# Optimization experiments

Measured on AMD Instinct MI355X. Metric: run time of the kernel, lower is better.

Reference implementation:

```python
import jax, jax.numpy as jnp
import numpy as np

NV, NS = 100000, 50000
DG, DS, H, OUT = 5, 6, 64, 8
EVV, EH, EIN, ESS = 1_000_000, 1_000_000, 500_000, 1_000_000


def _segsum(data, idx, n):
    return jax.ops.segment_sum(data, idx, num_segments=n)


def _edge_index(key, e, n_src, n_dst):
    k1, k2 = jax.random.split(key)
    return jnp.stack([
        jax.random.randint(k1, (e,), 0, n_src),
        jax.random.randint(k2, (e,), 0, n_dst),
    ]).astype(jnp.int64)


def setup_inputs() -> dict:
    key = jax.random.key(0)
    ks = jax.random.split(key, 16)
    s = 0.1
    inp = {
        "game_x": jax.random.normal(ks[0], (NV, DG), jnp.float32),
        "state_x": jax.random.normal(ks[1], (NS, DS), jnp.float32),
        "edge_index_v_v": _edge_index(ks[2], EVV, NV, NV),
        "edge_index_history_v_s": _edge_index(ks[3], EH, NV, NS),
        "edge_attr_history_v_s": jax.random.uniform(ks[4], (EH,), jnp.float32),
        "edge_index_in_v_s": _edge_index(ks[5], EIN, NV, NS),
        "edge_index_s_s": _edge_index(ks[6], ESS, NS, NS),
        # TAGConv(5, H, K=2): K+1 bias-free linears + bias
        "tag1_W": jax.random.normal(ks[7], (3, DG, H), jnp.float32) * s,
        "tag1_b": jnp.zeros((H,), jnp.float32),
        # TAGConv(H, H, K=3)
        "tag2_W": jax.random.normal(ks[8], (4, H, H), jnp.float32) * s,
        "tag2_b": jnp.zeros((H,), jnp.float32),
        # GraphConv((-1,-1), H): lin_rel (bias) + lin_root (no bias)
        "gc_W_rel": jax.random.normal(ks[9], (H, H), jnp.float32) * s,
        "gc_b": jnp.zeros((H,), jnp.float32),
        "gc_W_root": jax.random.normal(ks[10], (DS, H), jnp.float32) * s,
        # SAGEConv((-1,-1), H): lin_l (bias) + lin_r (no bias), mean aggr
        "sage_W_l": jax.random.normal(ks[11], (H, H), jnp.float32) * s,
        "sage_b_l": jnp.zeros((H,), jnp.float32),
        "sage_W_r": jax.random.normal(ks[12], (H, H), jnp.float32) * s,
        "lin_W": jax.random.normal(ks[13], (H, OUT), jnp.float32) * s,
        "lin_b": jnp.zeros((OUT,), jnp.float32),
    }
    return inp


def _tag_conv(x, edge_index, W, b):
    # TAGConv with gcn_norm (no self-loops): out = sum_k lin_k(A_hat^k x) + b
    n = x.shape[0]
    src, dst = edge_index[0], edge_index[1]
    deg = _segsum(jnp.ones(src.shape[0], x.dtype), dst, n)
    dinv = jnp.where(deg > 0, jax.lax.rsqrt(jnp.maximum(deg, 1e-12)), 0.0)
    norm = dinv[src] * dinv[dst]  # [E]
    out = x @ W[0]
    h = x
    for k in range(1, W.shape[0]):  # fixed, small K
        h = _segsum(h[src] * norm[:, None], dst, n)
        out = out + h @ W[k]
    return out + b


def _forward(game_x, state_x, edge_attr_history_v_s,
             tag1_W, tag1_b, tag2_W, tag2_b,
             gc_W_rel, gc_b, gc_W_root,
             sage_W_l, sage_b_l, sage_W_r, lin_W, lin_b,
             edge_index_v_v, edge_index_history_v_s,
             edge_index_in_v_s, edge_index_s_s):
    ns = state_x.shape[0]
    gx = jax.nn.relu(_tag_conv(game_x, edge_index_v_v, tag1_W, tag1_b))
    # GraphConv bipartite with edge weights: lin_rel(sum w*x_j) + lin_root(x_dst)
    src, dst = edge_index_history_v_s[0], edge_index_history_v_s[1]
    agg = _segsum(gx[src] * edge_attr_history_v_s[:, None], dst, ns)
    sx = jax.nn.relu(agg @ gc_W_rel + gc_b + state_x @ gc_W_root)
    # SAGEConv bipartite, mean aggr: lin_l(mean x_j) + lin_r(x_dst)
    src, dst = edge_index_in_v_s[0], edge_index_in_v_s[1]
    ssum = _segsum(gx[src], dst, ns)
    cnt = _segsum(jnp.ones(src.shape[0], gx.dtype), dst, ns)
    mean = ssum / jnp.maximum(cnt, 1.0)[:, None]
    sx = jax.nn.relu(mean @ sage_W_l + sage_b_l + sx @ sage_W_r)
    sx = jax.nn.relu(_tag_conv(sx, edge_index_s_s, tag2_W, tag2_b))
    return sx @ lin_W + lin_b


def reference(game_x, state_x, edge_index_v_v, edge_index_history_v_s,
              edge_attr_history_v_s, edge_index_in_v_s, edge_index_s_s,
              tag1_W, tag1_b, tag2_W, tag2_b, gc_W_rel, gc_b, gc_W_root,
              sage_W_l, sage_b_l, sage_W_r, lin_W, lin_b):
    return _forward(game_x, state_x, edge_attr_history_v_s,
                    tag1_W, tag1_b, tag2_W, tag2_b,
                    gc_W_rel, gc_b, gc_W_root,
                    sage_W_l, sage_b_l, sage_W_r, lin_W, lin_b,
                    edge_index_v_v, edge_index_history_v_s,
                    edge_index_in_v_s, edge_index_s_s)
```

## Files before the change

### kernel.cpp

```cpp
#include <hip/hip_runtime.h>

#define BLK 256
#define ACH 4096

__device__ __forceinline__ float bcast(float v, int l) {
    return __int_as_float(__builtin_amdgcn_readlane(__float_as_int(v), l));
}
__device__ __forceinline__ unsigned short f2bf(float f) {
    unsigned u = __float_as_uint(f);
    return (unsigned short)((u + 0x7FFFu + ((u >> 16) & 1u)) >> 16);
}
__device__ __forceinline__ float bf2f(unsigned short b) {
    return __uint_as_float(((unsigned)b) << 16);
}

typedef __attribute__((ext_vector_type(8))) short bf16x8;
typedef __attribute__((ext_vector_type(4))) float f32x4;

__device__ __forceinline__ void split8s(const float* p, float s, bf16x8& h, bf16x8& l) {
    #pragma unroll
    for (int j = 0; j < 8; j++) {
        float v = p[j] * s;
        unsigned short hb = f2bf(v);
        h[j] = (short)hb;
        l[j] = (short)f2bf(v - bf2f(hb));
    }
}
__device__ __forceinline__ void loadWsplit(const float* W, int kbase, int col,
                                           bf16x8& h, bf16x8& l) {
    #pragma unroll
    for (int j = 0; j < 8; j++) {
        float v = W[(size_t)(kbase + j) * 64 + col];
        unsigned short hb = f2bf(v);
        h[j] = (short)hb;
        l[j] = (short)f2bf(v - bf2f(hb));
    }
}


__global__ void k_binA1(const int* __restrict__ vd, const int* __restrict__ hd,
                        const int* __restrict__ id_, const int* __restrict__ sd,
                        int* __restrict__ Tv, int* __restrict__ Th,
                        int* __restrict__ Ti, int* __restrict__ Ts,
                        int ncv, int nch, int nci, int ncs,
                        int nbv_, int nbs_, int Ev, int Eh, int Ei, int Es) {
    __shared__ int cnt[512];
    int blk = blockIdx.x, t = threadIdx.x;
    const int* dd; int* T; int c, nc, nb, E, sf;
    if (blk < ncv)                 { dd = vd;  T = Tv; c = blk;               nc = ncv; nb = nbv_; E = Ev; sf = 8; }
    else if (blk < ncv + nch)      { dd = hd;  T = Th; c = blk - ncv;         nc = nch; nb = nbs_; E = Eh; sf = 7; }
    else if (blk < ncv + nch + nci){ dd = id_; T = Ti; c = blk - ncv - nch;   nc = nci; nb = nbs_; E = Ei; sf = 7; }
    else                           { dd = sd;  T = Ts; c = blk - ncv - nch - nci; nc = ncs; nb = nbs_; E = Es; sf = 7; }
    cnt[t] = 0; cnt[t + 256] = 0;
    __syncthreads();
    int p0 = c * ACH, p1 = min(E, p0 + ACH);
    for (int p = p0 + t; p < p1; p += 256) atomicAdd(&cnt[dd[p] >> sf], 1);
    __syncthreads();
    for (int b = t; b < nb; b += 256) T[(size_t)b * nc + c] = cnt[b];
}

__global__ void k_sb2(int* __restrict__ T, int* __restrict__ bsum,
                      int L0, int L1, int L2, int L3,
                      int nB0, int nB1, int nB2, int nB3) {
    __shared__ int sh[256];
    int blk = blockIdx.x;
    int lb, off, L;
    if (blk < nB0)                  { lb = blk;                 off = 0;            L = L0; }
    else if (blk < nB0 + nB1)       { lb = blk - nB0;           off = L0;           L = L1; }
    else if (blk < nB0 + nB1 + nB2) { lb = blk - nB0 - nB1;     off = L0 + L1;      L = L2; }
    else                            { lb = blk - nB0 - nB1 - nB2; off = L0 + L1 + L2; L = L3; }
    int i = lb * 256 + threadIdx.x;
    int v = (i < L) ? T[off + i] : 0;
    sh[threadIdx.x] = v; __syncthreads();
    for (int o2 = 1; o2 < 256; o2 <<= 1) {
        int tmp = (threadIdx.x >= o2) ? sh[threadIdx.x - o2] : 0;
        __syncthreads();
        sh[threadIdx.x] += tmp; __syncthreads();
    }
    if (i < L) T[off + i] = sh[threadIdx.x] - v;
    if (threadIdx.x == 255) bsum[blk] = sh[255];
}

__global__ void k_st2(int* __restrict__ bsum, int nB0, int nB1, int nB2, int nB3) {
    __shared__ int sh[1024];
    int g = blockIdx.x;
    int off = (g == 0) ? 0 : (g == 1) ? nB0 : (g == 2) ? nB0 + nB1 : nB0 + nB1 + nB2;
    int nb  = (g == 0) ? nB0 : (g == 1) ? nB1 : (g == 2) ? nB2 : nB3;
    int tid = threadIdx.x;
    int v = (tid < nb) ? bsum[off + tid] : 0;
    sh[tid] = v; __syncthreads();
    for (int o2 = 1; o2 < 1024; o2 <<= 1) {
        int t = (tid >= o2) ? sh[tid - o2] : 0;
        __syncthreads();
        sh[tid] += t; __syncthreads();
    }
    if (tid < nb) bsum[off + tid] = sh[tid] - v;
}

__global__ void k_sa2(int* __restrict__ T, const int* __restrict__ bsum,
                      int L0, int L1, int L2, int L3,
                      int nB0, int nB1, int nB2, int nB3) {
    int blk = blockIdx.x;
    int lb, off, L;
    if (blk < nB0)                  { lb = blk;                 off = 0;            L = L0; }
    else if (blk < nB0 + nB1)       { lb = blk - nB0;           off = L0;           L = L1; }
    else if (blk < nB0 + nB1 + nB2) { lb = blk - nB0 - nB1;     off = L0 + L1;      L = L2; }
    else                            { lb = blk - nB0 - nB1 - nB2; off = L0 + L1 + L2; L = L3; }
    int i = lb * 256 + threadIdx.x;
    if (i < L) T[off + i] += bsum[blk];
}

__global__ __launch_bounds__(512)
void k_binA2a(const int* __restrict__ vs, const int* __restrict__ vd,
              const int* __restrict__ is_, const int* __restrict__ id_,
              const int* __restrict__ ss_, const int* __restrict__ sd,
              const int* __restrict__ Tv, const int* __restrict__ Ti,
              const int* __restrict__ Ts,
              unsigned* __restrict__ vvbin, unsigned* __restrict__ inbin,
              unsigned* __restrict__ ssbin,
              int ncv, int nci, int ncs, int nbv_, int nbs_,
              int Ev, int Ei, int Es) {
    __shared__ int gbase[512], lscan[512], lcur[512];
    __shared__ unsigned sval[ACH];
    __shared__ int sdst[ACH];
    int blk = blockIdx.x, t = threadIdx.x;
    const int *srcp, *dstp, *T; unsigned* bin; int c, nc, nb, E, sf;
    if (blk < ncv)            { srcp = vs;  dstp = vd;  T = Tv; bin = vvbin; c = blk;             nc = ncv; nb = nbv_; E = Ev; sf = 8; }
    else if (blk < ncv + nci) { srcp = is_; dstp = id_; T = Ti; bin = inbin; c = blk - ncv;       nc = nci; nb = nbs_; E = Ei; sf = 7; }
    else                      { srcp = ss_; dstp = sd;  T = Ts; bin = ssbin; c = blk - ncv - nci; nc = ncs; nb = nbs_; E = Es; sf = 7; }
    int msk = (1 << sf) - 1;
    int p0 = c * ACH, p1 = min(E, p0 + ACH);
    if (t < nb) gbase[t] = T[(size_t)t * nc + c];
    lcur[t] = 0;
    int myS[8], myD[8];
    #pragma unroll
    for (int i = 0; i < 8; i++) {
        int p = p0 + t + i * 512;
        if (p < p1) { myS[i] = srcp[p]; myD[i] = dstp[p]; }
        else myD[i] = -1;
    }
    __syncthreads();
    #pragma unroll
    for (int i = 0; i < 8; i++)
        if (myD[i] >= 0) atomicAdd(&lcur[myD[i] >> sf], 1);
    __syncthreads();
    int v = lcur[t];
    lscan[t] = v;
    __syncthreads();
    for (int off = 1; off < 512; off <<= 1) {
        int tmp = (t >= off) ? lscan[t - off] : 0;
        __syncthreads();
        lscan[t] += tmp;
        __syncthreads();
    }
    int excl = lscan[t] - v;
    __syncthreads();
    lscan[t] = excl;
    lcur[t] = 0;
    __syncthreads();
    #pragma unroll
    for (int i = 0; i < 8; i++) {
        if (myD[i] < 0) continue;
        int b = myD[i] >> sf;
        int r = atomicAdd(&lcur[b], 1);
        int pos = lscan[b] + r;
        sval[pos] = ((unsigned)myS[i] << sf) | (unsigned)(myD[i] & msk);
        sdst[pos] = gbase[b] + r;
    }
    __syncthreads();
    int cntE = p1 - p0;
    for (int q = t; q < cntE; q += 512) bin[sdst[q]] = sval[q];
}

__global__ __launch_bounds__(512)
void k_binA2h(const int* __restrict__ hs, const int* __restrict__ hd,
              const float* __restrict__ hw, const int* __restrict__ Th,
              int2* __restrict__ hbin, int nch, int nbs_, int Eh) {
    __shared__ int gbase[512], lscan[512], lcur[512];
    __shared__ unsigned sval[ACH];
    __shared__ int sdst[ACH];
    __shared__ float swt[ACH];
    int c = blockIdx.x, t = threadIdx.x;
    const int sf = 7, msk = 127;
    int p0 = c * ACH, p1 = min(Eh, p0 + ACH);
    if (t < nbs_) gbase[t] = Th[(size_t)t * nch + c];
    lcur[t] = 0;
    int myS[8], myD[8]; float myW[8];
    #pragma unroll
    for (int i = 0; i < 8; i++) {
        int p = p0 + t + i * 512;
        if (p < p1) { myS[i] = hs[p]; myD[i] = hd[p]; myW[i] = hw[p]; }
        else myD[i] = -1;
    }
    __syncthreads();
    #pragma unroll
    for (int i = 0; i < 8; i++)
        if (myD[i] >= 0) atomicAdd(&lcur[myD[i] >> sf], 1);
    __syncthreads();
    int v = lcur[t];
    lscan[t] = v;
    __syncthreads();
    for (int off = 1; off < 512; off <<= 1) {
        int tmp = (t >= off) ? lscan[t - off] : 0;
        __syncthreads();
        lscan[t] += tmp;
        __syncthreads();
    }
    int excl = lscan[t] - v;
    __syncthreads();
    lscan[t] = excl;
    lcur[t] = 0;
    __syncthreads();
    #pragma unroll
    for (int i = 0; i < 8; i++) {
        if (myD[i] < 0) continue;
        int b = myD[i] >> sf;
        int r = atomicAdd(&lcur[b], 1);
        int pos = lscan[b] + r;
        sval[pos] = ((unsigned)myS[i] << sf) | (unsigned)(myD[i] & msk);
        sdst[pos] = gbase[b] + r;
        swt[pos] = myW[i];
    }
    __syncthreads();
    int cntE = p1 - p0;
    for (int q = t; q < cntE; q += 512)
        hbin[sdst[q]] = make_int2((int)sval[q], __float_as_int(swt[q]));
}

__global__ void k_binB(const unsigned* __restrict__ vvbin, const int2* __restrict__ hbin,
                       const unsigned* __restrict__ inbin, const unsigned* __restrict__ ssbin,
                       const int* __restrict__ Tv, const int* __restrict__ Th,
                       const int* __restrict__ Ti, const int* __restrict__ Ts,
                       int* __restrict__ rv, int* __restrict__ rh,
                       int* __restrict__ ri, int* __restrict__ rs,
                       float* __restrict__ dinv_v, float* __restrict__ dinv_s,
                       int* __restrict__ vvsrc, int2* __restrict__ hsw,
                       int* __restrict__ insrc, int* __restrict__ sssrc,
                       int ncv, int nch, int nci, int ncs,
                       int nbv_, int nbs_, int nv, int ns,
                       int Ev, int Eh, int Ei, int Es) {
    __shared__ int cnt[256]; __shared__ int pre[256]; __shared__ int cur[256];
    int blk = blockIdx.x, t = threadIdx.x;
    int g, b, nb, nc, sf, n, E; const int* T; int* rp;
    if (blk < nbv_)                 { g = 0; b = blk;                 nb = nbv_; nc = ncv; sf = 8; n = nv; E = Ev; T = Tv; rp = rv; }
    else if (blk < nbv_ + nbs_)     { g = 1; b = blk - nbv_;          nb = nbs_; nc = nch; sf = 7; n = ns; E = Eh; T = Th; rp = rh; }
    else if (blk < nbv_ + 2 * nbs_) { g = 2; b = blk - nbv_ - nbs_;   nb = nbs_; nc = nci; sf = 7; n = ns; E = Ei; T = Ti; rp = ri; }
    else                            { g = 3; b = blk - nbv_ - 2 * nbs_; nb = nbs_; nc = ncs; sf = 7; n = ns; E = Es; T = Ts; rp = rs; }
    int W = 1 << sf, msk = W - 1;
    int e0 = T[(size_t)b * nc];
    int e1 = (b + 1 < nb) ? T[(size_t)(b + 1) * nc] : E;
    cnt[t] = 0; __syncthreads();
    for (int p = e0 + t; p < e1; p += 256) {
        unsigned pk = (g == 1) ? (unsigned)hbin[p].x
                    : (g == 0) ? vvbin[p] : (g == 2) ? inbin[p] : ssbin[p];
        atomicAdd(&cnt[pk & msk], 1);
    }
    __syncthreads();
    int v = cnt[t];
    pre[t] = v; __syncthreads();
    for (int o2 = 1; o2 < 256; o2 <<= 1) {
        int tmp = (t >= o2) ? pre[t - o2] : 0;
        __syncthreads();
        pre[t] += tmp; __syncthreads();
    }
    int excl = pre[t] - v;
    int d = b * W + t;
    if (t < W && d < n) {
        rp[d] = e0 + excl;
        if (g == 0)      dinv_v[d] = v > 0 ? rsqrtf((float)v) : 0.f;
        else if (g == 3) dinv_s[d] = v > 0 ? rsqrtf((float)v) : 0.f;
    }
    cur[t] = e0 + excl;
    __syncthreads();
    for (int p = e0 + t; p < e1; p += 256) {
        if (g == 1) {
            int2 r = hbin[p];
            unsigned pk = (unsigned)r.x;
            int pos = atomicAdd(&cur[pk & msk], 1);
            hsw[pos] = make_int2((int)(pk >> sf), r.y);
        } else {
            unsigned pk = (g == 0) ? vvbin[p] : (g == 2) ? inbin[p] : ssbin[p];
            int pos = atomicAdd(&cur[pk & msk], 1);
            int sv = (int)(pk >> sf);
            if (g == 0)      vvsrc[pos] = sv;
            else if (g == 2) insrc[pos] = sv;
            else             sssrc[pos] = sv;
        }
    }
    if (b == 0 && t == 0) rp[n] = E;
}


__global__ void k_pack5(const float* __restrict__ x, const float* __restrict__ dinv,
                        float* __restrict__ P, int n) {
    int i = blockIdx.x * blockDim.x + threadIdx.x;
    if (i >= n) return;
    const float* xp = x + (size_t)i * 5;
    float4 a = make_float4(xp[0], xp[1], xp[2], xp[3]);
    float4 b = make_float4(xp[4], dinv[i], 0.f, 0.f);
    ((float4*)P)[(size_t)i * 2]     = a;
    ((float4*)P)[(size_t)i * 2 + 1] = b;
}

__global__ void k_gather5p(const float* __restrict__ Pin, const int* __restrict__ rowptr,
                           const int* __restrict__ csr_src, float* __restrict__ Pout, int n) {
    int d = blockIdx.x * blockDim.x + threadIdx.x;
    if (d >= n) return;
    int b = rowptr[d], e = rowptr[d + 1];
    float dd = Pin[(size_t)d * 8 + 5];
    float a0 = 0, a1 = 0, a2 = 0, a3 = 0, a4 = 0;
    int p = b;
    for (; p + 4 <= e; p += 4) {
        int s0 = csr_src[p], s1 = csr_src[p+1], s2 = csr_src[p+2], s3 = csr_src[p+3];
        float4 x0a = ((const float4*)Pin)[(size_t)s0 * 2], x0b = ((const float4*)Pin)[(size_t)s0 * 2 + 1];
        float4 x1a = ((const float4*)Pin)[(size_t)s1 * 2], x1b = ((const float4*)Pin)[(size_t)s1 * 2 + 1];
        float4 x2a = ((const float4*)Pin)[(size_t)s2 * 2], x2b = ((const float4*)Pin)[(size_t)s2 * 2 + 1];
        float4 x3a = ((const float4*)Pin)[(size_t)s3 * 2], x3b = ((const float4*)Pin)[(size_t)s3 * 2 + 1];
        float w0 = dd * x0b.y, w1 = dd * x1b.y, w2 = dd * x2b.y, w3 = dd * x3b.y;
        a0 += x0a.x*w0 + x1a.x*w1 + x2a.x*w2 + x3a.x*w3;
        a1 += x0a.y*w0 + x1a.y*w1 + x2a.y*w2 + x3a.y*w3;
        a2 += x0a.z*w0 + x1a.z*w1 + x2a.z*w2 + x3a.z*w3;
        a3 += x0a.w*w0 + x1a.w*w1 + x2a.w*w2 + x3a.w*w3;
        a4 += x0b.x*w0 + x1b.x*w1 + x2b.x*w2 + x3b.x*w3;
    }
    for (; p < e; p++) {
        int s = csr_src[p];
        float4 xa = ((const float4*)Pin)[(size_t)s * 2], xb = ((const float4*)Pin)[(size_t)s * 2 + 1];
        float w = dd * xb.y;
        a0 += xa.x*w; a1 += xa.y*w; a2 += xa.z*w; a3 += xa.w*w; a4 += xb.x*w;
    }
    ((float4*)Pout)[(size_t)d * 2]     = make_float4(a0, a1, a2, a3);
    ((float4*)Pout)[(size_t)d * 2 + 1] = make_float4(a4, dd, 0.f, 0.f);
}

template<int MODE, bool OUTBF>
__global__ void k_gather64(const unsigned short* __restrict__ xbf, const int* __restrict__ rowptr,
                           const int* __restrict__ csr_src, const int2* __restrict__ csr_sw,
                           const float* __restrict__ dinv, void* __restrict__ outp, int n) {
    int wid = (int)(((long long)blockIdx.x * blockDim.x + threadIdx.x) >> 6);
    if (wid >= n) return;
    int lane = threadIdx.x & 63;
    int g = lane >> 4, q = lane & 15;
    int b = rowptr[wid], e = rowptr[wid + 1];
    float dd = (MODE == 2) ? dinv[wid] : 0.f;
    float4 acc = make_float4(0.f, 0.f, 0.f, 0.f);
    int p = b + g;
    for (; p + 12 < e; p += 16) {
        int s0, s1, s2, s3;
        float w0 = 1.f, w1 = 1.f, w2 = 1.f, w3 = 1.f;
        if (MODE == 1) {
            int2 e0 = csr_sw[p], e1 = csr_sw[p+4], e2 = csr_sw[p+8], e3 = csr_sw[p+12];
            s0 = e0.x; w0 = __int_as_float(e0.y);
            s1 = e1.x; w1 = __int_as_float(e1.y);
            s2 = e2.x; w2 = __int_as_float(e2.y);
            s3 = e3.x; w3 = __int_as_float(e3.y);
        } else {
            s0 = csr_src[p]; s1 = csr_src[p+4]; s2 = csr_src[p+8]; s3 = csr_src[p+12];
            if (MODE == 2) {
                w0 = dd * dinv[s0]; w1 = dd * dinv[s1];
                w2 = dd * dinv[s2]; w3 = dd * dinv[s3];
            }
        }
        ushort4 u0 = ((const ushort4*)(xbf + (size_t)s0 * 64))[q];
        ushort4 u1 = ((const ushort4*)(xbf + (size_t)s1 * 64))[q];
        ushort4 u2 = ((const ushort4*)(xbf + (size_t)s2 * 64))[q];
        ushort4 u3 = ((const ushort4*)(xbf + (size_t)s3 * 64))[q];
        acc.x += bf2f(u0.x)*w0 + bf2f(u1.x)*w1 + bf2f(u2.x)*w2 + bf2f(u3.x)*w3;
        acc.y += bf2f(u0.y)*w0 + bf2f(u1.y)*w1 + bf2f(u2.y)*w2 + bf2f(u3.y)*w3;
        acc.z += bf2f(u0.z)*w0 + bf2f(u1.z)*w1 + bf2f(u2.z)*w2 + bf2f(u3.z)*w3;
        acc.w += bf2f(u0.w)*w0 + bf2f(u1.w)*w1 + bf2f(u2.w)*w2 + bf2f(u3.w)*w3;
    }
    for (; p < e; p += 4) {
        int s; float w = 1.f;
        if (MODE == 1) { int2 e0 = csr_sw[p]; s = e0.x; w = __int_as_float(e0.y); }
        else { s = csr_src[p]; if (MODE == 2) w = dd * dinv[s]; }
        ushort4 u = ((const ushort4*)(xbf + (size_t)s * 64))[q];
        acc.x += bf2f(u.x)*w; acc.y += bf2f(u.y)*w;
        acc.z += bf2f(u.z)*w; acc.w += bf2f(u.w)*w;
    }
    #pragma unroll
    for (int off = 16; off < 64; off <<= 1) {
        acc.x += __shfl_xor(acc.x, off, 64);
        acc.y += __shfl_xor(acc.y, off, 64);
        acc.z += __shfl_xor(acc.z, off, 64);
        acc.w += __shfl_xor(acc.w, off, 64);
    }
    if (g == 0) {
        if (OUTBF) {
            ushort4 ov;
            ov.x = f2bf(acc.x); ov.y = f2bf(acc.y); ov.z = f2bf(acc.z); ov.w = f2bf(acc.w);
            ((ushort4*)outp)[(size_t)wid * 16 + q] = ov;
        } else {
            ((float4*)outp)[(size_t)wid * 16 + q] = acc;
        }
    }
}


__global__ __launch_bounds__(256)
void k_sage_mf(const float* __restrict__ ssum, const int* __restrict__ rp,
               const float* __restrict__ sx, const float* __restrict__ Wl,
               const float* __restrict__ Wr, const float* __restrict__ bl,
               unsigned short* __restrict__ out, int n) {
    int wv = (int)(((long long)blockIdx.x * blockDim.x + threadIdx.x) >> 6);
    int lane = threadIdx.x & 63;
    int r0 = wv * 32;
    if (r0 >= n) return;
    int lm = lane & 15, g = lane >> 4;
    bf16x8 axh[2][2], axl[2][2], ayh[2][2], ayl[2][2];
    #pragma unroll
    for (int mt = 0; mt < 2; mt++) {
        int row = r0 + mt * 16 + lm; if (row >= n) row = n - 1;
        float cnt = (float)(rp[row + 1] - rp[row]);
        float rs = 1.f / fmaxf(cnt, 1.f);
        #pragma unroll
        for (int kh = 0; kh < 2; kh++) {
            split8s(ssum + (size_t)row * 64 + kh * 32 + g * 8, rs,  axh[mt][kh], axl[mt][kh]);
            split8s(sx   + (size_t)row * 64 + kh * 32 + g * 8, 1.f, ayh[mt][kh], ayl[mt][kh]);
        }
    }
    #pragma unroll
    for (int nt = 0; nt < 4; nt++) {
        int col = nt * 16 + lm;
        bf16x8 blh[2], bll[2], brh[2], brl[2];
        #pragma unroll
        for (int kh = 0; kh < 2; kh++) {
            loadWsplit(Wl, kh * 32 + g * 8, col, blh[kh], bll[kh]);
            loadWsplit(Wr, kh * 32 + g * 8, col, brh[kh], brl[kh]);
        }
        #pragma unroll
        for (int mt = 0; mt < 2; mt++) {
            f32x4 acc = {0.f, 0.f, 0.f, 0.f};
            #pragma unroll
            for (int kh = 0; kh < 2; kh++) {
                acc = __builtin_amdgcn_mfma_f32_16x16x32_bf16(axh[mt][kh], blh[kh], acc, 0, 0, 0);
                acc = __builtin_amdgcn_mfma_f32_16x16x32_bf16(axl[mt][kh], blh[kh], acc, 0, 0, 0);
                acc = __builtin_amdgcn_mfma_f32_16x16x32_bf16(axh[mt][kh], bll[kh], acc, 0, 0, 0);
                acc = __builtin_amdgcn_mfma_f32_16x16x32_bf16(ayh[mt][kh], brh[kh], acc, 0, 0, 0);
                acc = __builtin_amdgcn_mfma_f32_16x16x32_bf16(ayl[mt][kh], brh[kh], acc, 0, 0, 0);
                acc = __builtin_amdgcn_mfma_f32_16x16x32_bf16(ayh[mt][kh], brl[kh], acc, 0, 0, 0);
            }
            #pragma unroll
            for (int r = 0; r < 4; r++) {
                int row = r0 + mt * 16 + g * 4 + r;
                if (row < n)
                    out[(size_t)row * 64 + col] = f2bf(fmaxf(bl[col] + acc[r], 0.f));
            }
        }
    }
}

__global__ __launch_bounds__(256)
void k_gc_mf(const float* __restrict__ agg, const float* __restrict__ st,
             const float* __restrict__ Wrel, const float* __restrict__ Wroot,
             const float* __restrict__ b, float* __restrict__ out, int n) {
    int wv = (int)(((long long)blockIdx.x * blockDim.x + threadIdx.x) >> 6);
    int lane = threadIdx.x & 63;
    int r0 = wv * 32;
    if (r0 >= n) return;
    int lm = lane & 15, g = lane >> 4;
    bf16x8 axh[2][2], axl[2][2], arh[2], arl[2];
    #pragma unroll
    for (int mt = 0; mt < 2; mt++) {
        int row = r0 + mt * 16 + lm; if (row >= n) row = n - 1;
        #pragma unroll
        for (int kh = 0; kh < 2; kh++)
            split8s(agg + (size_t)row * 64 + kh * 32 + g * 8, 1.f, axh[mt][kh], axl[mt][kh]);
        #pragma unroll
        for (int j = 0; j < 8; j++) {
            int k = g * 8 + j;
            float v = (k < 6) ? st[(size_t)row * 6 + k] : 0.f;
            unsigned short hb = f2bf(v);
            arh[mt][j] = (short)hb;
            arl[mt][j] = (short)f2bf(v - bf2f(hb));
        }
    }
    #pragma unroll
    for (int nt = 0; nt < 4; nt++) {
        int col = nt * 16 + lm;
        bf16x8 bh[2], blo[2], brh, brl;
        #pragma unroll
        for (int kh = 0; kh < 2; kh++) loadWsplit(Wrel, kh * 32 + g * 8, col, bh[kh], blo[kh]);
        #pragma unroll
        for (int j = 0; j < 8; j++) {
            int k = g * 8 + j;
            float v = (k < 6) ? Wroot[(size_t)k * 64 + col] : 0.f;
            unsigned short hb = f2bf(v);
            brh[j] = (short)hb;
            brl[j] = (short)f2bf(v - bf2f(hb));
        }
        #pragma unroll
        for (int mt = 0; mt < 2; mt++) {
            f32x4 acc = {0.f, 0.f, 0.f, 0.f};
            #pragma unroll
            for (int kh = 0; kh < 2; kh++) {
                acc = __builtin_amdgcn_mfma_f32_16x16x32_bf16(axh[mt][kh], bh[kh],  acc, 0, 0, 0);
                acc = __builtin_amdgcn_mfma_f32_16x16x32_bf16(axl[mt][kh], bh[kh],  acc, 0, 0, 0);
                acc = __builtin_amdgcn_mfma_f32_16x16x32_bf16(axh[mt][kh], blo[kh], acc, 0, 0, 0);
            }
            acc = __builtin_amdgcn_mfma_f32_16x16x32_bf16(arh[mt], brh, acc, 0, 0, 0);
            acc = __builtin_amdgcn_mfma_f32_16x16x32_bf16(arl[mt], brh, acc, 0, 0, 0);
            acc = __builtin_amdgcn_mfma_f32_16x16x32_bf16(arh[mt], brl, acc, 0, 0, 0);
            #pragma unroll
            for (int r = 0; r < 4; r++) {
                int row = r0 + mt * 16 + g * 4 + r;
                if (row < n)
                    out[(size_t)row * 64 + col] = fmaxf(b[col] + acc[r], 0.f);
            }
        }
    }
}

__global__ __launch_bounds__(256)
void k_tagmm(const unsigned short* __restrict__ x0, const unsigned short* __restrict__ x1,
             const unsigned short* __restrict__ x2, const unsigned short* __restrict__ x3,
             const float* __restrict__ W4, const float* __restrict__ tb,
             const float* __restrict__ lW, const float* __restrict__ lb,
             float* __restrict__ out, int n) {
    __shared__ float lds[4][32][64];
    int tid = threadIdx.x;
    int wv = (int)(((long long)blockIdx.x * blockDim.x + tid) >> 6);
    int w = (tid >> 6) & 3;
    int lane = tid & 63;
    int lm = lane & 15, g = lane >> 4;
    int r0 = wv * 32;
    bool active = (r0 < n);
    int r0c = active ? r0 : 0;
    const unsigned short* xs[4] = {x0, x1, x2, x3};
    f32x4 acc[2][4];
    #pragma unroll
    for (int mt = 0; mt < 2; mt++)
        #pragma unroll
        for (int nt = 0; nt < 4; nt++) acc[mt][nt] = (f32x4){0.f, 0.f, 0.f, 0.f};
    #pragma unroll
    for (int inp = 0; inp < 4; inp++) {
        const unsigned short* xp = xs[inp];
        const float* W = W4 + inp * 4096;
        bf16x8 a[2][2];
        #pragma unroll
        for (int mt = 0; mt < 2; mt++) {
            int row = r0c + mt * 16 + lm; if (row >= n) row = n - 1;
            #pragma unroll
            for (int kh = 0; kh < 2; kh++)
                a[mt][kh] = *(const bf16x8*)(xp + (size_t)row * 64 + kh * 32 + g * 8);
        }
        #pragma unroll
        for (int nt = 0; nt < 4; nt++) {
            int col = nt * 16 + lm;
            bf16x8 bh[2], blo[2];
            #pragma unroll
            for (int kh = 0; kh < 2; kh++) loadWsplit(W, kh * 32 + g * 8, col, bh[kh], blo[kh]);
            #pragma unroll
            for (int mt = 0; mt < 2; mt++) {
                #pragma unroll
                for (int kh = 0; kh < 2; kh++) {
                    acc[mt][nt] = __builtin_amdgcn_mfma_f32_16x16x32_bf16(a[mt][kh], bh[kh],  acc[mt][nt], 0, 0, 0);
                    acc[mt][nt] = __builtin_amdgcn_mfma_f32_16x16x32_bf16(a[mt][kh], blo[kh], acc[mt][nt], 0, 0, 0);
                }
            }
        }
    }
    #pragma unroll
    for (int mt = 0; mt < 2; mt++)
        #pragma unroll
        for (int nt = 0; nt < 4; nt++) {
            int col = nt * 16 + lm;
            float bias = tb[col];
            #pragma unroll
            for (int r = 0; r < 4; r++)
                lds[w][mt * 16 + g * 4 + r][col] = fmaxf(bias + acc[mt][nt][r], 0.f);
        }
    __syncthreads();
    bf16x8 bh2[2], bl2[2];
    #pragma unroll
    for (int kh = 0; kh < 2; kh++) {
        #pragma unroll
        for (int j = 0; j < 8; j++) {
            int k = kh * 32 + g * 8 + j;
            float v = (lm < 8) ? lW[k * 8 + lm] : 0.f;
            unsigned short hb = f2bf(v);
            bh2[kh][j] = (short)hb;
            bl2[kh][j] = (short)f2bf(v - bf2f(hb));
        }
    }
    #pragma unroll
    for (int mt = 0; mt < 2; mt++) {
        bf16x8 ah[2], al[2];
        #pragma unroll
        for (int kh = 0; kh < 2; kh++) {
            #pragma unroll
            for (int j = 0; j < 8; j++) {
                float v = lds[w][mt * 16 + lm][kh * 32 + g * 8 + j];
                unsigned short hb = f2bf(v);
                ah[kh][j] = (short)hb;
                al[kh][j] = (short)f2bf(v - bf2f(hb));
            }
        }
        f32x4 oacc = {0.f, 0.f, 0.f, 0.f};
        #pragma unroll
        for (int kh = 0; kh < 2; kh++) {
            oacc = __builtin_amdgcn_mfma_f32_16x16x32_bf16(ah[kh], bh2[kh], oacc, 0, 0, 0);
            oacc = __builtin_amdgcn_mfma_f32_16x16x32_bf16(al[kh], bh2[kh], oacc, 0, 0, 0);
            oacc = __builtin_amdgcn_mfma_f32_16x16x32_bf16(ah[kh], bl2[kh], oacc, 0, 0, 0);
        }
        if (lm < 8) {
            #pragma unroll
            for (int r = 0; r < 4; r++) {
                int row = r0 + mt * 16 + g * 4 + r;
                if (active && row < n) out[(size_t)row * 8 + lm] = oacc[r] + lb[lm];
            }
        }
    }
}

__global__ __launch_bounds__(256, 4)
void k_tag1_w(const float* __restrict__ x, const float* __restrict__ h1,
              const float* __restrict__ h2, const float* __restrict__ W,
              const float* __restrict__ b, unsigned short* __restrict__ out, int n) {
    int wv = (int)(((long long)blockIdx.x * blockDim.x + threadIdx.x) >> 6);
    int lane = threadIdx.x & 63;
    int i0 = wv * 4;
    if (i0 >= n) return;
    float v[4], acc[4];
    #pragma unroll
    for (int r = 0; r < 4; r++) {
        int i = (i0 + r < n) ? i0 + r : n - 1;
        float t = 0.f;
        if (lane < 5)                     t = x [(size_t)i * 5 + lane];
        else if (lane >= 8 && lane < 13)  t = h1[(size_t)i * 8 + lane - 8];
        else if (lane >= 16 && lane < 21) t = h2[(size_t)i * 8 + lane - 16];
        v[r] = t;
        acc[r] = b[lane];
    }
    #pragma unroll
    for (int m = 0; m < 3; m++) {
        #pragma unroll
        for (int k = 0; k < 5; k++) {
            float wk = W[(m * 5 + k) * 64 + lane];
            #pragma unroll
            for (int r = 0; r < 4; r++) acc[r] += bcast(v[r], m * 8 + k) * wk;
        }
    }
    #pragma unroll
    for (int r = 0; r < 4; r++)
        if (i0 + r < n) out[(size_t)(i0 + r) * 64 + lane] = f2bf(fmaxf(acc[r], 0.f));
}

static inline unsigned gblk(long long n) { return (unsigned)((n + BLK - 1) / BLK); }
static inline unsigned gwv4(long long n) { return gblk(((n + 3) / 4) * 64); }
static inline unsigned gw32(long long n) { return gblk(((n + 31) / 32) * 64); }

extern "C" void kernel_launch(void* const* d_in, const int* in_sizes, int n_in,
                              void* d_out, int out_size, void* d_ws, size_t ws_size,
                              hipStream_t stream) {
    const float* game_x  = (const float*)d_in[0];
    const float* state_x = (const float*)d_in[1];
    const int*   ei_vv   = (const int*)d_in[2];
    const int*   ei_h    = (const int*)d_in[3];
    const float* ea_h    = (const float*)d_in[4];
    const int*   ei_in   = (const int*)d_in[5];
    const int*   ei_ss   = (const int*)d_in[6];
    const float* tag1_W  = (const float*)d_in[7];
    const float* tag1_b  = (const float*)d_in[8];
    const float* tag2_W  = (const float*)d_in[9];
    const float* tag2_b  = (const float*)d_in[10];
    const float* gc_Wrel = (const float*)d_in[11];
    const float* gc_b    = (const float*)d_in[12];
    const float* gc_Wroot= (const float*)d_in[13];
    const float* sage_Wl = (const float*)d_in[14];
    const float* sage_bl = (const float*)d_in[15];
    const float* sage_Wr = (const float*)d_in[16];
    const float* lin_W   = (const float*)d_in[17];
    const float* lin_b   = (const float*)d_in[18];

    const int NV  = in_sizes[0] / 5;
    const int NS  = in_sizes[1] / 6;
    const int EVV = in_sizes[2] / 2;
    const int EH  = in_sizes[3] / 2;
    const int EIN = in_sizes[5] / 2;
    const int ESS = in_sizes[6] / 2;

    const int *vv_s = ei_vv,  *vv_d = ei_vv + EVV;
    const int *h_s  = ei_h,   *h_d  = ei_h  + EH;
    const int *in_s = ei_in,  *in_d = ei_in + EIN;
    const int *ss_s = ei_ss,  *ss_d = ei_ss + ESS;

    const int ncv = (EVV + ACH - 1) / ACH;
    const int nch = (EH  + ACH - 1) / ACH;
    const int nci = (EIN + ACH - 1) / ACH;
    const int ncs = (ESS + ACH - 1) / ACH;
    const int nbv_ = (NV + 255) >> 8;
    const int nbs_ = (NS + 127) >> 7;
    const int Lv = nbv_ * ncv, Lh = nbs_ * nch, Li = nbs_ * nci, Ls = nbs_ * ncs;
    const int nB0 = (Lv + 255) / 256, nB1 = (Lh + 255) / 256,
              nB2 = (Li + 255) / 256, nB3 = (Ls + 255) / 256;

    float* wsf = (float*)d_ws;
    size_t o = 0;
    unsigned short* gx_bf = (unsigned short*)(wsf + o);
    o += (size_t)NV * 32;
    float* B1 = wsf + o; o += (size_t)NS * 64;
    float* B2 = wsf + o; o += (size_t)NS * 64;
    float* B4 = wsf + o; o += (size_t)NS * 32;
    float* B5 = wsf + o; o += (size_t)NS * 32;
    int*  vvsrc = (int*)(wsf + o); o += (size_t)EVV;
    int*  sssrc = (int*)(wsf + o); o += (size_t)ESS;
    int*  insrc = (int*)(wsf + o); o += (size_t)EIN;
    int2* hsw   = (int2*)(wsf + o); o += (size_t)EH * 2;
    int* T_all = (int*)(wsf + o); o += (size_t)(Lv + Lh + Li + Ls);
    int* bsum  = (int*)(wsf + o); o += 2048;
    int* rv = (int*)(wsf + o); o += (size_t)NV + 1;
    int* rh = (int*)(wsf + o); o += (size_t)NS + 1;
    int* ri = (int*)(wsf + o); o += (size_t)NS + 1;
    int* rs = (int*)(wsf + o); o += (size_t)NS + 1;
    float* dinv_v = wsf + o; o += (size_t)NV;
    float* dinv_s = wsf + o; o += (size_t)NS;

    int* Tv = T_all;
    int* Th = Tv + Lv;
    int* Ti = Th + Lh;
    int* Ts = Ti + Li;

    unsigned* vvbin = (unsigned*)B1;
    unsigned* inbin = vvbin + EVV;
    unsigned* ssbin = inbin + EIN;
    int2* hbin = (int2*)B2;

    unsigned short* hA_bf  = (unsigned short*)B1;
    unsigned short* hB_bf  = (unsigned short*)B2;
    unsigned short* hC_bf  = (unsigned short*)B5;
    unsigned short* sx2_bf = (unsigned short*)B4;
    float* P0 = B5;
    float* H1 = B4;
    float* H2 = B4 + (size_t)NV * 8;

    int nbins   = nbv_ + 3 * nbs_;
    int nBtot   = nB0 + nB1 + nB2 + nB3;
    k_binA1<<<ncv + nch + nci + ncs, 256, 0, stream>>>(vv_d, h_d, in_d, ss_d, Tv, Th, Ti, Ts,
                                         ncv, nch, nci, ncs, nbv_, nbs_,
                                         EVV, EH, EIN, ESS);
    k_sb2<<<nBtot, 256, 0, stream>>>(T_all, bsum, Lv, Lh, Li, Ls, nB0, nB1, nB2, nB3);
    k_st2<<<4, 1024, 0, stream>>>(bsum, nB0, nB1, nB2, nB3);
    k_sa2<<<nBtot, 256, 0, stream>>>(T_all, bsum, Lv, Lh, Li, Ls, nB0, nB1, nB2, nB3);
    k_binA2a<<<ncv + nci + ncs, 512, 0, stream>>>(vv_s, vv_d, in_s, in_d, ss_s, ss_d,
                                                  Tv, Ti, Ts, vvbin, inbin, ssbin,
                                                  ncv, nci, ncs, nbv_, nbs_,
                                                  EVV, EIN, ESS);
    k_binA2h<<<nch, 512, 0, stream>>>(h_s, h_d, ea_h, Th, hbin, nch, nbs_, EH);
    k_binB<<<nbins, 256, 0, stream>>>(vvbin, hbin, inbin, ssbin,
                                      Tv, Th, Ti, Ts,
                                      rv, rh, ri, rs, dinv_v, dinv_s,
                                      vvsrc, hsw, insrc, sssrc,
                                      ncv, nch, nci, ncs, nbv_, nbs_,
                                      NV, NS, EVV, EH, EIN, ESS);

    k_pack5<<<gblk(NV), BLK, 0, stream>>>(game_x, dinv_v, P0, NV);
    k_gather5p<<<gblk(NV), BLK, 0, stream>>>(P0, rv, vvsrc, H1, NV);
    k_gather5p<<<gblk(NV), BLK, 0, stream>>>(H1, rv, vvsrc, H2, NV);
    k_tag1_w<<<gwv4(NV), BLK, 0, stream>>>(game_x, H1, H2, tag1_W, tag1_b, gx_bf, NV);

    k_gather64<1, false><<<gblk((long long)NS * 64), BLK, 0, stream>>>(gx_bf, rh, nullptr, hsw, nullptr, B1, NS);
    k_gc_mf<<<gw32(NS), BLK, 0, stream>>>(B1, state_x, gc_Wrel, gc_Wroot, gc_b, B2, NS);

    k_gather64<0, false><<<gblk((long long)NS * 64), BLK, 0, stream>>>(gx_bf, ri, insrc, nullptr, nullptr, B1, NS);
    k_sage_mf<<<gw32(NS), BLK, 0, stream>>>(B1, ri, B2, sage_Wl, sage_Wr, sage_bl, sx2_bf, NS);

    k_gather64<2, true><<<gblk((long long)NS * 64), BLK, 0, stream>>>(sx2_bf, rs, sssrc, nullptr, dinv_s, hA_bf, NS);
    k_gather64<2, true><<<gblk((long long)NS * 64), BLK, 0, stream>>>(hA_bf, rs, sssrc, nullptr, dinv_s, hB_bf, NS);
    k_gather64<2, true><<<gblk((long long)NS * 64), BLK, 0, stream>>>(hB_bf, rs, sssrc, nullptr, dinv_s, hC_bf, NS);
    k_tagmm<<<gw32(NS), BLK, 0, stream>>>(sx2_bf, hA_bf, hB_bf, hC_bf,
                                          tag2_W, tag2_b, lin_W, lin_b,
                                          (float*)d_out, NS);
}
```

Before: 395.6 us.

## Fuse pack into binning, merge GC/SAGE gathers and matmuls into fewer kernels

Folds the game_x packing and dinv computation into the CSR-building k_binB kernel, removing k_pack5 and the dinv_v buffer. The history and in-edge gathers now run in a single launch (k_gatherBC), with the first half of the waves handling history and the second half in-edges. GraphConv and SAGE matmuls are fused into one kernel that keeps the intermediate state features in LDS instead of writing them to global memory. This cuts launch count and intermediate global traffic, at the cost of 32KB LDS per block, which may lower occupancy, and a block-wide sync.

New measurement: 411.4 us. 4.0% more time.

```diff
diff --git a/kernel.cpp b/kernel.cpp
--- a/kernel.cpp
+++ b/kernel.cpp
@@ -233,7 +233,8 @@
                        const int* __restrict__ Ti, const int* __restrict__ Ts,
                        int* __restrict__ rv, int* __restrict__ rh,
                        int* __restrict__ ri, int* __restrict__ rs,
-                       float* __restrict__ dinv_v, float* __restrict__ dinv_s,
+                       const float* __restrict__ gx5, float* __restrict__ P0,
+                       float* __restrict__ dinv_s,
                        int* __restrict__ vvsrc, int2* __restrict__ hsw,
                        int* __restrict__ insrc, int* __restrict__ sssrc,
                        int ncv, int nch, int nci, int ncs,
@@ -267,8 +268,14 @@
     int d = b * W + t;
     if (t < W && d < n) {
         rp[d] = e0 + excl;
-        if (g == 0)      dinv_v[d] = v > 0 ? rsqrtf((float)v) : 0.f;
-        else if (g == 3) dinv_s[d] = v > 0 ? rsqrtf((float)v) : 0.f;
+        if (g == 0) {
+            const float* xp = gx5 + (size_t)d * 5;
+            float di = v > 0 ? rsqrtf((float)v) : 0.f;
+            ((float4*)P0)[(size_t)d * 2]     = make_float4(xp[0], xp[1], xp[2], xp[3]);
+            ((float4*)P0)[(size_t)d * 2 + 1] = make_float4(xp[4], di, 0.f, 0.f);
+        } else if (g == 3) {
+            dinv_s[d] = v > 0 ? rsqrtf((float)v) : 0.f;
+        }
     }
     cur[t] = e0 + excl;
     __syncthreads();
@@ -290,17 +297,6 @@
     if (b == 0 && t == 0) rp[n] = E;
 }
 
-
-__global__ void k_pack5(const float* __restrict__ x, const float* __restrict__ dinv,
-                        float* __restrict__ P, int n) {
-    int i = blockIdx.x * blockDim.x + threadIdx.x;
-    if (i >= n) return;
-    const float* xp = x + (size_t)i * 5;
-    float4 a = make_float4(xp[0], xp[1], xp[2], xp[3]);
-    float4 b = make_float4(xp[4], dinv[i], 0.f, 0.f);
-    ((float4*)P)[(size_t)i * 2]     = a;
-    ((float4*)P)[(size_t)i * 2 + 1] = b;
-}
 
 __global__ void k_gather5p(const float* __restrict__ Pin, const int* __restrict__ rowptr,
                            const int* __restrict__ csr_src, float* __restrict__ Pout, int n) {
@@ -331,6 +327,75 @@
     }
     ((float4*)Pout)[(size_t)d * 2]     = make_float4(a0, a1, a2, a3);
     ((float4*)Pout)[(size_t)d * 2 + 1] = make_float4(a4, dd, 0.f, 0.f);
+}
+
+__global__ void k_gatherBC(const unsigned short* __restrict__ xbf,
+                           const int* __restrict__ rh, const int2* __restrict__ hsw,
+                           const int* __restrict__ ri, const int* __restrict__ insrc,
+                           float* __restrict__ aggH, float* __restrict__ aggI, int n) {
+    int wid = (int)(((long long)blockIdx.x * blockDim.x + threadIdx.x) >> 6);
+    if (wid >= 2 * n) return;
+    int lane = threadIdx.x & 63;
+    int g = lane >> 4, q = lane & 15;
+    float4 acc = make_float4(0.f, 0.f, 0.f, 0.f);
+    float* outp;
+    int row;
+    if (wid < n) {
+        row = wid;
+        int b = rh[row], e = rh[row + 1];
+        int p = b + g;
+        for (; p + 12 < e; p += 16) {
+            int2 e0 = hsw[p], e1 = hsw[p+4], e2 = hsw[p+8], e3 = hsw[p+12];
+            float w0 = __int_as_float(e0.y), w1 = __int_as_float(e1.y);
+            float w2 = __int_as_float(e2.y), w3 = __int_as_float(e3.y);
+            ushort4 u0 = ((const ushort4*)(xbf + (size_t)e0.x * 64))[q];
+            ushort4 u1 = ((const ushort4*)(xbf + (size_t)e1.x * 64))[q];
+            ushort4 u2 = ((const ushort4*)(xbf + (size_t)e2.x * 64))[q];
+            ushort4 u3 = ((const ushort4*)(xbf + (size_t)e3.x * 64))[q];
+            acc.x += bf2f(u0.x)*w0 + bf2f(u1.x)*w1 + bf2f(u2.x)*w2 + bf2f(u3.x)*w3;
+            acc.y += bf2f(u0.y)*w0 + bf2f(u1.y)*w1 + bf2f(u2.y)*w2 + bf2f(u3.y)*w3;
+            acc.z += bf2f(u0.z)*w0 + bf2f(u1.z)*w1 + bf2f(u2.z)*w2 + bf2f(u3.z)*w3;
+            acc.w += bf2f(u0.w)*w0 + bf2f(u1.w)*w1 + bf2f(u2.w)*w2 + bf2f(u3.w)*w3;
+        }
+        for (; p < e; p += 4) {
+            int2 e0 = hsw[p];
+            float w = __int_as_float(e0.y);
+            ushort4 u = ((const ushort4*)(xbf + (size_t)e0.x * 64))[q];
+            acc.x += bf2f(u.x)*w; acc.y += bf2f(u.y)*w;
+            acc.z += bf2f(u.z)*w; acc.w += bf2f(u.w)*w;
+        }
+        outp = aggH;
+    } else {
+        row = wid - n;
+        int b = ri[row], e = ri[row + 1];
+        int p = b + g;
+        for (; p + 12 < e; p += 16) {
+            int s0 = insrc[p], s1 = insrc[p+4], s2 = insrc[p+8], s3 = insrc[p+12];
+            ushort4 u0 = ((const ushort4*)(xbf + (size_t)s0 * 64))[q];
+            ushort4 u1 = ((const ushort4*)(xbf + (size_t)s1 * 64))[q];
+            ushort4 u2 = ((const ushort4*)(xbf + (size_t)s2 * 64))[q];
+            ushort4 u3 = ((const ushort4*)(xbf + (size_t)s3 * 64))[q];
+            acc.x += bf2f(u0.x) + bf2f(u1.x) + bf2f(u2.x) + bf2f(u3.x);
+            acc.y += bf2f(u0.y) + bf2f(u1.y) + bf2f(u2.y) + bf2f(u3.y);
+            acc.z += bf2f(u0.z) + bf2f(u1.z) + bf2f(u2.z) + bf2f(u3.z);
+            acc.w += bf2f(u0.w) + bf2f(u1.w) + bf2f(u2.w) + bf2f(u3.w);
+        }
+        for (; p < e; p += 4) {
+            int s = insrc[p];
+            ushort4 u = ((const ushort4*)(xbf + (size_t)s * 64))[q];
+            acc.x += bf2f(u.x); acc.y += bf2f(u.y);
+            acc.z += bf2f(u.z); acc.w += bf2f(u.w);
+        }
+        outp = aggI;
+    }
+    #pragma unroll
+    for (int off = 16; off < 64; off <<= 1) {
+        acc.x += __shfl_xor(acc.x, off, 64);
+        acc.y += __shfl_xor(acc.y, off, 64);
+        acc.z += __shfl_xor(acc.z, off, 64);
+        acc.w += __shfl_xor(acc.w, off, 64);
+    }
+    if (g == 0) ((float4*)outp)[(size_t)row * 16 + q] = acc;
 }
 
 template<int MODE, bool OUTBF>
@@ -398,114 +463,120 @@
 
 
 __global__ __launch_bounds__(256)
-void k_sage_mf(const float* __restrict__ ssum, const int* __restrict__ rp,
-               const float* __restrict__ sx, const float* __restrict__ Wl,
-               const float* __restrict__ Wr, const float* __restrict__ bl,
-               unsigned short* __restrict__ out, int n) {
-    int wv = (int)(((long long)blockIdx.x * blockDim.x + threadIdx.x) >> 6);
-    int lane = threadIdx.x & 63;
+void k_gcsage_mf(const float* __restrict__ aggH, const float* __restrict__ st,
+                 const float* __restrict__ Wrel, const float* __restrict__ Wroot,
+                 const float* __restrict__ gb,
+                 const float* __restrict__ ssum, const int* __restrict__ ri,
+                 const float* __restrict__ Wl, const float* __restrict__ Wr,
+                 const float* __restrict__ sbl,
+                 unsigned short* __restrict__ out, int n) {
+    __shared__ float lds[4][32][64];
+    int tid = threadIdx.x;
+    int wv = (int)(((long long)blockIdx.x * blockDim.x + tid) >> 6);
+    int w = (tid >> 6) & 3;
+    int lane = tid & 63;
+    int lm = lane & 15, g = lane >> 4;
     int r0 = wv * 32;
-    if (r0 >= n) return;
-    int lm = lane & 15, g = lane >> 4;
-    bf16x8 axh[2][2], axl[2][2], ayh[2][2], ayl[2][2];
-    #pragma unroll
-    for (int mt = 0; mt < 2; mt++) {
-        int row = r0 + mt * 16 + lm; if (row >= n) row = n - 1;
-        float cnt = (float)(rp[row + 1] - rp[row]);
-        float rs = 1.f / fmaxf(cnt, 1.f);
-        #pragma unroll
-        for (int kh = 0; kh < 2; kh++) {
-            split8s(ssum + (size_t)row * 64 + kh * 32 + g * 8, rs,  axh[mt][kh], axl[mt][kh]);
-            split8s(sx   + (size_t)row * 64 + kh * 32 + g * 8, 1.f, ayh[mt][kh], ayl[mt][kh]);
-        }
-    }
-    #pragma unroll
-    for (int nt = 0; nt < 4; nt++) {
-        int col = nt * 16 + lm;
-        bf16x8 blh[2], bll[2], brh[2], brl[2];
-        #pragma unroll
-        for (int kh = 0; kh < 2; kh++) {
-            loadWsplit(Wl, kh * 32 + g * 8, col, blh[kh], bll[kh]);
-            loadWsplit(Wr, kh * 32 + g * 8, col, brh[kh], brl[kh]);
-        }
+    bool active = (r0 < n);
+    int r0c = active ? r0 : 0;
+    {
+        bf16x8 axh[2][2], axl[2][2], arh[2], arl[2];
         #pragma unroll
         for (int mt = 0; mt < 2; mt++) {
-            f32x4 acc = {0.f, 0.f, 0.f, 0.f};
+            int row = r0c + mt * 16 + lm; if (row >= n) row = n - 1;
+            #pragma unroll
+            for (int kh = 0; kh < 2; kh++)
+                split8s(aggH + (size_t)row * 64 + kh * 32 + g * 8, 1.f, axh[mt][kh], axl[mt][kh]);
+            #pragma unroll
+            for (int j = 0; j < 8; j++) {
+                int k = g * 8 + j;
+                float v = (k < 6) ? st[(size_t)row * 6 + k] : 0.f;
+                unsigned short hb = f2bf(v);
+                arh[mt][j] = (short)hb;
+                arl[mt][j] = (short)f2bf(v - bf2f(hb));
+            }
+        }
+        #pragma unroll
+        for (int nt = 0; nt < 4; nt++) {
+            int col = nt * 16 + lm;
+            bf16x8 bh[2], blo[2], brh, brl;
+            #pragma unroll
+            for (int kh = 0; kh < 2; kh++) loadWsplit(Wrel, kh * 32 + g * 8, col, bh[kh], blo[kh]);
+            #pragma unroll
+            for (int j = 0; j < 8; j++) {
+                int k = g * 8 + j;
+                float v = (k < 6) ? Wroot[(size_t)k * 64 + col] : 0.f;
+                unsigned short hb = f2bf(v);
+                brh[j] = (short)hb;
+                brl[j] = (short)f2bf(v - bf2f(hb));
+            }
+            #pragma unroll
+            for (int mt = 0; mt < 2; mt++) {
+                f32x4 acc = {0.f, 0.f, 0.f, 0.f};
+                #pragma unroll
+                for (int kh = 0; kh < 2; kh++) {
+                    acc = __builtin_amdgcn_mfma_f32_16x16x32_bf16(axh[mt][kh], bh[kh],  acc, 0, 0, 0);
+                    acc = __builtin_amdgcn_mfma_f32_16x16x32_bf16(axl[mt][kh], bh[kh],  acc, 0, 0, 0);
+                    acc = __builtin_amdgcn_mfma_f32_16x16x32_bf16(axh[mt][kh], blo[kh], acc, 0, 0, 0);
+                }
+                acc = __builtin_amdgcn_mfma_f32_16x16x32_bf16(arh[mt], brh, acc, 0, 0, 0);
+                acc = __builtin_amdgcn_mfma_f32_16x16x32_bf16(arl[mt], brh, acc, 0, 0, 0);
+                acc = __builtin_amdgcn_mfma_f32_16x16x32_bf16(arh[mt], brl, acc, 0, 0, 0);
+                float bias = gb[col];
+                #pragma unroll
+                for (int r = 0; r < 4; r++)
+                    lds[w][mt * 16 + g * 4 + r][col] = fmaxf(bias + acc[r], 0.f);
+            }
+        }
+    }
+    __syncthreads();
+    {
+        bf16x8 mh[2][2], ml[2][2], sh_[2][2], sl_[2][2];
+        #pragma unroll
+        for (int mt = 0; mt < 2; mt++) {
+            int row = r0c + mt * 16 + lm; if (row >= n) row = n - 1;
+            float cnt = (float)(ri[row + 1] - ri[row]);
+            float rs = 1.f / fmaxf(cnt, 1.f);
             #pragma unroll
             for (int kh = 0; kh < 2; kh++) {
-                acc = __builtin_amdgcn_mfma_f32_16x16x32_bf16(axh[mt][kh], blh[kh], acc, 0, 0, 0);
-                acc = __builtin_amdgcn_mfma_f32_16x16x32_bf16(axl[mt][kh], blh[kh], acc, 0, 0, 0);
-                acc = __builtin_amdgcn_mfma_f32_16x16x32_bf16(axh[mt][kh], bll[kh], acc, 0, 0, 0);
-                acc = __builtin_amdgcn_mfma_f32_16x16x32_bf16(ayh[mt][kh], brh[kh], acc, 0, 0, 0);
-                acc = __builtin_amdgcn_mfma_f32_16x16x32_bf16(ayl[mt][kh], brh[kh], acc, 0, 0, 0);
-                acc = __builtin_amdgcn_mfma_f32_16x16x32_bf16(ayh[mt][kh], brl[kh], acc, 0, 0, 0);
-            }
-            #pragma unroll
-            for (int r = 0; r < 4; r++) {
-                int row = r0 + mt * 16 + g * 4 + r;
-                if (row < n)
-                    out[(size_t)row * 64 + col] = f2bf(fmaxf(bl[col] + acc[r], 0.f));
-            }
-        }
-    }
-}
-
-__global__ __launch_bounds__(256)
-void k_gc_mf(const float* __restrict__ agg, const float* __restrict__ st,
-             const float* __restrict__ Wrel, const float* __restrict__ Wroot,
-             const float* __restrict__ b, float* __restrict__ out, int n) {
-    int wv = (int)(((long long)blockIdx.x * blockDim.x + threadIdx.x) >> 6);
-    int lane = threadIdx.x & 63;
-    int r0 = wv * 32;
-    if (r0 >= n) return;
-    int lm = lane & 15, g = lane >> 4;
-    bf16x8 axh[2][2], axl[2][2], arh[2], arl[2];
-    #pragma unroll
-    for (int mt = 0; mt < 2; mt++) {
-        int row = r0 + mt * 16 + lm; if (row >= n) row = n - 1;
-        #pragma unroll
-        for (int kh = 0; kh < 2; kh++)
-            split8s(agg + (size_t)row * 64 + kh * 32 + g * 8, 1.f, axh[mt][kh], axl[mt][kh]);
-        #pragma unroll
-        for (int j = 0; j < 8; j++) {
-            int k = g * 8 + j;
-            float v = (k < 6) ? st[(size_t)row * 6 + k] : 0.f;
-            unsigned short hb = f2bf(v);
-            arh[mt][j] = (short)hb;
-            arl[mt][j] = (short)f2bf(v - bf2f(hb));
-        }
-    }
-    #pragma unroll
-    for (int nt = 0; nt < 4; nt++) {
-        int col = nt * 16 + lm;
-        bf16x8 bh[2], blo[2], brh, brl;
-        #pragma unroll
-        for (int kh = 0; kh < 2; kh++) loadWsplit(Wrel, kh * 32 + g * 8, col, bh[kh], blo[kh]);
-        #pragma unroll
-        for (int j = 0; j < 8; j++) {
-            int k = g * 8 + j;
-            float v = (k < 6) ? Wroot[(size_t)k * 64 + col] : 0.f;
-            unsigned short hb = f2bf(v);
-            brh[j] = (short)hb;
-            brl[j] = (short)f2bf(v - bf2f(hb));
-        }
-        #pragma unroll
-        for (int mt = 0; mt < 2; mt++) {
-            f32x4 acc = {0.f, 0.f, 0.f, 0.f};
+                split8s(ssum + (size_t)row * 64 + kh * 32 + g * 8, rs, mh[mt][kh], ml[mt][kh]);
+                #pragma unroll
+                for (int j = 0; j < 8; j++) {
+                    float v = lds[w][mt * 16 + lm][kh * 32 + g * 8 + j];
+                    unsigned short hb = f2bf(v);
+                    sh_[mt][kh][j] = (short)hb;
+                    sl_[mt][kh][j] = (short)f2bf(v - bf2f(hb));
+                }
+            }
+        }
+        #pragma unroll
+        for (int nt = 0; nt < 4; nt++) {
+            int col = nt * 16 + lm;
+            bf16x8 blh[2], bll[2], brh2[2], brl2[2];
             #pragma unroll
             for (int kh = 0; kh < 2; kh++) {
-                acc = __builtin_amdgcn_mfma_f32_16x16x32_bf16(axh[mt][kh], bh[kh],  acc, 0, 0, 0);
-                acc = __builtin_amdgcn_mfma_f32_16x16x32_bf16(axl[mt][kh], bh[kh],  acc, 0, 0, 0);
-                acc = __builtin_amdgcn_mfma_f32_16x16x32_bf16(axh[mt][kh], blo[kh], acc, 0, 0, 0);
-            }
-            acc = __builtin_amdgcn_mfma_f32_16x16x32_bf16(arh[mt], brh, acc, 0, 0, 0);
-            acc = __builtin_amdgcn_mfma_f32_16x16x32_bf16(arl[mt], brh, acc, 0, 0, 0);
-            acc = __builtin_amdgcn_mfma_f32_16x16x32_bf16(arh[mt], brl, acc, 0, 0, 0);
-            #pragma unroll
-            for (int r = 0; r < 4; r++) {
-                int row = r0 + mt * 16 + g * 4 + r;
-                if (row < n)
-                    out[(size_t)row * 64 + col] = fmaxf(b[col] + acc[r], 0.f);
+                loadWsplit(Wl, kh * 32 + g * 8, col, blh[kh], bll[kh]);
+                loadWsplit(Wr, kh * 32 + g * 8, col, brh2[kh], brl2[kh]);
+            }
+            #pragma unroll
+            for (int mt = 0; mt < 2; mt++) {
+                f32x4 acc = {0.f, 0.f, 0.f, 0.f};
+                #pragma unroll
+                for (int kh = 0; kh < 2; kh++) {
+                    acc = __builtin_amdgcn_mfma_f32_16x16x32_bf16(mh[mt][kh],  blh[kh],  acc, 0, 0, 0);
+                    acc = __builtin_amdgcn_mfma_f32_16x16x32_bf16(ml[mt][kh],  blh[kh],  acc, 0, 0, 0);
+                    acc = __builtin_amdgcn_mfma_f32_16x16x32_bf16(mh[mt][kh],  bll[kh],  acc, 0, 0, 0);
+                    acc = __builtin_amdgcn_mfma_f32_16x16x32_bf16(sh_[mt][kh], brh2[kh], acc, 0, 0, 0);
+                    acc = __builtin_amdgcn_mfma_f32_16x16x32_bf16(sl_[mt][kh], brh2[kh], acc, 0, 0, 0);
+                    acc = __builtin_amdgcn_mfma_f32_16x16x32_bf16(sh_[mt][kh], brl2[kh], acc, 0, 0, 0);
+                }
+                float bias = sbl[col];
+                #pragma unroll
+                for (int r = 0; r < 4; r++) {
+                    int row = r0 + mt * 16 + g * 4 + r;
+                    if (active && row < n)
+                        out[(size_t)row * 64 + col] = f2bf(fmaxf(bias + acc[r], 0.f));
+                }
             }
         }
     }
@@ -713,7 +784,6 @@
     int* rh = (int*)(wsf + o); o += (size_t)NS + 1;
     int* ri = (int*)(wsf + o); o += (size_t)NS + 1;
     int* rs = (int*)(wsf + o); o += (size_t)NS + 1;
-    float* dinv_v = wsf + o; o += (size_t)NV;
     float* dinv_s = wsf + o; o += (size_t)NS;
 
     int* Tv = T_all;
@@ -749,21 +819,21 @@
     k_binA2h<<<nch, 512, 0, stream>>>(h_s, h_d, ea_h, Th, hbin, nch, nbs_, EH);
     k_binB<<<nbins, 256, 0, stream>>>(vvbin, hbin, inbin, ssbin,
                                       Tv, Th, Ti, Ts,
-                                      rv, rh, ri, rs, dinv_v, dinv_s,
+                                      rv, rh, ri, rs,
+                                      game_x, P0, dinv_s,
                                       vvsrc, hsw, insrc, sssrc,
                                       ncv, nch, nci, ncs, nbv_, nbs_,
                                       NV, NS, EVV, EH, EIN, ESS);
 
-    k_pack5<<<gblk(NV), BLK, 0, stream>>>(game_x, dinv_v, P0, NV);
     k_gather5p<<<gblk(NV), BLK, 0, stream>>>(P0, rv, vvsrc, H1, NV);
     k_gather5p<<<gblk(NV), BLK, 0, stream>>>(H1, rv, vvsrc, H2, NV);
     k_tag1_w<<<gwv4(NV), BLK, 0, stream>>>(game_x, H1, H2, tag1_W, tag1_b, gx_bf, NV);
 
-    k_gather64<1, false><<<gblk((long long)NS * 64), BLK, 0, stream>>>(gx_bf, rh, nullptr, hsw, nullptr, B1, NS);
-    k_gc_mf<<<gw32(NS), BLK, 0, stream>>>(B1, state_x, gc_Wrel, gc_Wroot, gc_b, B2, NS);
-
-    k_gather64<0, false><<<gblk((long long)NS * 64), BLK, 0, stream>>>(gx_bf, ri, insrc, nullptr, nullptr, B1, NS);
-    k_sage_mf<<<gw32(NS), BLK, 0, stream>>>(B1, ri, B2, sage_Wl, sage_Wr, sage_bl, sx2_bf, NS);
+    k_gatherBC<<<gblk(2LL * NS * 64), BLK, 0, stream>>>(gx_bf, rh, hsw, ri, insrc,
+                                                        B1, B2, NS);
+    k_gcsage_mf<<<gw32(NS), BLK, 0, stream>>>(B1, state_x, gc_Wrel, gc_Wroot, gc_b,
+                                              B2, ri, sage_Wl, sage_Wr, sage_bl,
+                                              sx2_bf, NS);
 
     k_gather64<2, true><<<gblk((long long)NS * 64), BLK, 0, stream>>>(sx2_bf, rs, sssrc, nullptr, dinv_s, hA_bf, NS);
     k_gather64<2, true><<<gblk((long long)NS * 64), BLK, 0, stream>>>(hA_bf, rs, sssrc, nullptr, dinv_s, hB_bf, NS);
```
